# Performance work log

Measured on AMD Instinct MI355X. Metric: run time of the kernel, lower is better.

Reference implementation:

```python
import jax, jax.numpy as jnp
import numpy as np

B, T, I, H, O = 64, 2048, 128, 256, 128


def setup_inputs() -> dict:
    key = jax.random.key(0)
    ks = jax.random.split(key, 7)
    s_xh = 1.0 / np.sqrt(I)
    s_hh = 1.0 / np.sqrt(H)
    return {
        "x": jax.random.normal(ks[0], (B, T, I), dtype=jnp.float32),
        "h0": jax.random.normal(ks[1], (B, H), dtype=jnp.float32),
        "Wxh": jax.random.uniform(ks[2], (H, I), jnp.float32, -s_xh, s_xh),
        "Whh": jax.random.uniform(ks[3], (H, H), jnp.float32, -s_hh, s_hh),
        "bh": jax.random.uniform(ks[4], (H,), jnp.float32, -s_hh, s_hh),
        "Wout": jax.random.uniform(ks[5], (O, H), jnp.float32, -s_hh, s_hh),
        "bout": jax.random.uniform(ks[6], (O,), jnp.float32, -s_hh, s_hh),
    }


def reference(x, h0, Wxh, Whh, bh, Wout, bout):
    # x: (B, T, I) -> scan over time with hidden state h: (B, H)
    def step(h, xt):
        # Elman cell: h' = tanh(x Wxh^T + h Whh^T + b)
        h_new = jnp.tanh(xt @ Wxh.T + h @ Whh.T + bh)
        y = h_new @ Wout.T + bout  # (B, O) per-step output head
        return h_new, y

    xT = jnp.swapaxes(x, 0, 1)  # (T, B, I)
    hT, Ys = jax.lax.scan(step, h0, xT)
    Y = jnp.swapaxes(Ys, 0, 1)  # (B, T, O)
    return Y, hT
```

## Files before the change

### kernel.cpp

```cpp
#include <hip/hip_runtime.h>
#include <hip/hip_bf16.h>
#include <hip/hip_fp16.h>

#define B_SZ 64
#define T_SZ 2048
#define I_SZ 128
#define H_SZ 256
#define O_SZ 128

typedef _Float16 half_t;
typedef _Float16 h2_t __attribute__((ext_vector_type(2)));
typedef _Float16 h8_t __attribute__((ext_vector_type(8)));
typedef float    f4_t __attribute__((ext_vector_type(4)));

static __device__ __forceinline__ h2_t uint_as_h2(unsigned u) {
  union { unsigned u; h2_t h; } x; x.u = u; return x.h;
}
static __device__ __forceinline__ unsigned pack_h2(float a, float b) {
  h2_t h; h[0] = (_Float16)a; h[1] = (_Float16)b;
  union { h2_t h; unsigned u; } x; x.h = h; return x.u;
}
static __device__ __forceinline__ float dot2(h2_t a, h2_t b, float c) {
#if __has_builtin(__builtin_amdgcn_fdot2)
  return __builtin_amdgcn_fdot2(a, b, c, false);
#else
  return c + (float)a[0] * (float)b[0] + (float)a[1] * (float)b[1];
#endif
}
static __device__ __forceinline__ float fast_rcp(float x) {
#if __has_builtin(__builtin_amdgcn_rcpf)
  return __builtin_amdgcn_rcpf(x);
#else
  return 1.0f / x;
#endif
}

template <int BM, int BN, int BK, int KTOT, bool A_HALF, bool OUT_HALF>
__global__ __launch_bounds__(256, 2) void gemm_tn_bias(
    const void* __restrict__ Ap, const float* __restrict__ Bw,
    const float* __restrict__ bias, void* __restrict__ Out, int ldo) {
  extern __shared__ half_t lds[];
  half_t* As = lds;
  half_t* Bs = lds + BM * BK;

  const int tid = threadIdx.x;
  const long row0 = (long)blockIdx.x * BM;
  const int col0 = blockIdx.y * BN;

  constexpr int MI = 4;
  constexpr int NJ = (BN / 2) / 16;
  const int lane = tid & 63, wid = tid >> 6;
  const int wm = (wid >> 1) * 64;
  const int wn = (wid & 1) * (BN / 2);

  f4_t acc[MI][NJ];
#pragma unroll
  for (int mi = 0; mi < MI; ++mi)
#pragma unroll
    for (int nj = 0; nj < NJ; ++nj) acc[mi][nj] = (f4_t){0.f, 0.f, 0.f, 0.f};

#pragma unroll 1
  for (int kt = 0; kt < KTOT / BK; ++kt) {
    if (kt) __syncthreads();
    constexpr int AIT = (BM * BK) / (256 * 8);
#pragma unroll
    for (int it = 0; it < AIT; ++it) {
      int idx = (it * 256 + tid) * 8;
      int r = idx / BK, c = idx % BK;
      uint4 v;
      if (A_HALF) {
        v = *(const uint4*)((const half_t*)Ap + (row0 + r) * (long)KTOT +
                            kt * BK + c);
      } else {
        const float* src =
            (const float*)Ap + (row0 + r) * (long)KTOT + kt * BK + c;
        float4 f0 = *(const float4*)(src);
        float4 f1 = *(const float4*)(src + 4);
        v.x = pack_h2(f0.x, f0.y); v.y = pack_h2(f0.z, f0.w);
        v.z = pack_h2(f1.x, f1.y); v.w = pack_h2(f1.z, f1.w);
      }
      int chunk = (c >> 3) ^ (r & 7);
      *(uint4*)(&As[r * BK + chunk * 8]) = v;
    }
    constexpr int BIT = (BN * BK) / (256 * 8);
#pragma unroll
    for (int it = 0; it < BIT; ++it) {
      int idx = (it * 256 + tid) * 8;
      int r = idx / BK, c = idx % BK;
      const float* src = Bw + (long)(col0 + r) * KTOT + kt * BK + c;
      float4 f0 = *(const float4*)(src);
      float4 f1 = *(const float4*)(src + 4);
      uint4 v;
      v.x = pack_h2(f0.x, f0.y); v.y = pack_h2(f0.z, f0.w);
      v.z = pack_h2(f1.x, f1.y); v.w = pack_h2(f1.z, f1.w);
      int chunk = (c >> 3) ^ (r & 7);
      *(uint4*)(&Bs[r * BK + chunk * 8]) = v;
    }
    __syncthreads();

#pragma unroll
    for (int ks = 0; ks < BK / 32; ++ks) {
      h8_t af[MI], bf[NJ];
#pragma unroll
      for (int mi = 0; mi < MI; ++mi) {
        int r = wm + mi * 16 + (lane & 15);
        int chunk = (ks * 4 + (lane >> 4)) ^ (r & 7);
        af[mi] = *(const h8_t*)(&As[r * BK + chunk * 8]);
      }
#pragma unroll
      for (int nj = 0; nj < NJ; ++nj) {
        int r = wn + nj * 16 + (lane & 15);
        int chunk = (ks * 4 + (lane >> 4)) ^ (r & 7);
        bf[nj] = *(const h8_t*)(&Bs[r * BK + chunk * 8]);
      }
#pragma unroll
      for (int mi = 0; mi < MI; ++mi)
#pragma unroll
        for (int nj = 0; nj < NJ; ++nj)
          acc[mi][nj] = __builtin_amdgcn_mfma_f32_16x16x32_f16(
              af[mi], bf[nj], acc[mi][nj], 0, 0, 0);
    }
  }

#pragma unroll
  for (int mi = 0; mi < MI; ++mi) {
#pragma unroll
    for (int nj = 0; nj < NJ; ++nj) {
#pragma unroll
      for (int e = 0; e < 4; ++e) {
        long row = row0 + wm + mi * 16 + (lane >> 4) * 4 + e;
        int col = col0 + wn + nj * 16 + (lane & 15);
        float val = acc[mi][nj][e] + bias[col];
        if (OUT_HALF)
          ((half_t*)Out)[row * ldo + col] = (half_t)val;
        else
          ((float*)Out)[row * ldo + col] = val;
      }
    }
  }
}

__global__ __launch_bounds__(256, 1) void rnn_scan(
    const half_t* __restrict__ Xp,
    const float* __restrict__ Whh,
    const float* __restrict__ h0,
    half_t* __restrict__ Hs,
    float* __restrict__ hT) {
  __shared__ __align__(16) unsigned short hbuf[2][H_SZ];
  const int tid = threadIdx.x;
  const int b = blockIdx.x;
  const int q = tid & 3;
  const int g = tid >> 2;

  unsigned wpk[4][32];
#pragma unroll
  for (int r = 0; r < 4; ++r) {
    const float* wrow = Whh + (4 * g + r) * H_SZ + q * 64;
#pragma unroll
    for (int i = 0; i < 16; ++i) {
      float4 f = *(const float4*)(wrow + i * 4);
      wpk[r][2 * i] = pack_h2(f.x, f.y);
      wpk[r][2 * i + 1] = pack_h2(f.z, f.w);
    }
  }
  {
    union { _Float16 h; unsigned short s; } cv;
    cv.h = (_Float16)h0[b * H_SZ + tid];
    hbuf[0][tid] = cv.s;
  }
  __syncthreads();

  const half_t* xp = Xp + (long)b * T_SZ * H_SZ + tid;
  half_t* hs = Hs + (long)b * T_SZ * H_SZ + tid;
  float* hTo = hT + b * H_SZ + tid;

  half_t xv = xp[0];
#pragma unroll 1
  for (int t = 0; t < T_SZ; ++t) {
    half_t xnxt = (t + 1 < T_SZ) ? xp[(long)(t + 1) * H_SZ] : (half_t)0.0f;
    const int cur = t & 1;
    const uint4* hp = (const uint4*)(&hbuf[cur][q * 64]);
    float a0 = 0.f, a1 = 0.f, a2 = 0.f, a3 = 0.f;
#pragma unroll
    for (int i = 0; i < 8; ++i) {
      uint4 v = hp[i];
      unsigned hv0 = v.x, hv1 = v.y, hv2 = v.z, hv3 = v.w;
#define DOT_STEP(c, hvu)                                     \
  {                                                          \
    h2_t hh = uint_as_h2(hvu);                               \
    a0 = dot2(uint_as_h2(wpk[0][i * 4 + c]), hh, a0);        \
    a1 = dot2(uint_as_h2(wpk[1][i * 4 + c]), hh, a1);        \
    a2 = dot2(uint_as_h2(wpk[2][i * 4 + c]), hh, a2);        \
    a3 = dot2(uint_as_h2(wpk[3][i * 4 + c]), hh, a3);        \
  }
      DOT_STEP(0, hv0) DOT_STEP(1, hv1) DOT_STEP(2, hv2) DOT_STEP(3, hv3)
#undef DOT_STEP
    }
    a0 += __shfl_xor(a0, 1); a0 += __shfl_xor(a0, 2);
    a1 += __shfl_xor(a1, 1); a1 += __shfl_xor(a1, 2);
    a2 += __shfl_xor(a2, 1); a2 += __shfl_xor(a2, 2);
    a3 += __shfl_xor(a3, 1); a3 += __shfl_xor(a3, 2);
    float a = (q == 0) ? a0 : (q == 1) ? a1 : (q == 2) ? a2 : a3;
    a += (float)xv;
    float ex = __expf(2.0f * a);
    float hn = 1.0f - 2.0f * fast_rcp(ex + 1.0f);

    hs[(long)t * H_SZ] = (half_t)hn;
    if (t == T_SZ - 1) *hTo = hn;
    {
      union { _Float16 h; unsigned short s; } cv;
      cv.h = (_Float16)hn;
      hbuf[cur ^ 1][tid] = cv.s;
    }
    xv = xnxt;
    __syncthreads();
  }
}

extern "C" void kernel_launch(void* const* d_in, const int* in_sizes, int n_in,
                              void* d_out, int out_size, void* d_ws,
                              size_t ws_size, hipStream_t stream) {
  const float* x = (const float*)d_in[0];
  const float* h0 = (const float*)d_in[1];
  const float* Wxh = (const float*)d_in[2];
  const float* Whh = (const float*)d_in[3];
  const float* bh = (const float*)d_in[4];
  const float* Wout = (const float*)d_in[5];
  const float* bout = (const float*)d_in[6];

  half_t* Xp = (half_t*)d_out;
  half_t* Hs = (half_t*)d_ws;
  float* Y = (float*)d_out;
  float* hT = (float*)d_out + (long)B_SZ * T_SZ * O_SZ;

  const long M = (long)B_SZ * T_SZ;

  {
    dim3 grid((unsigned)(M / 128), H_SZ / 128);
    size_t sh = 2ull * 128 * 128 * sizeof(half_t);
    hipLaunchKernelGGL((gemm_tn_bias<128, 128, 128, 128, false, true>), grid,
                       dim3(256), sh, stream, (const void*)x, Wxh, bh,
                       (void*)Xp, H_SZ);
  }
  hipLaunchKernelGGL(rnn_scan, dim3(B_SZ), dim3(256), 0, stream, Xp, Whh, h0,
                     Hs, hT);
  {
    dim3 grid((unsigned)(M / 128), O_SZ / 128);
    size_t sh = 2ull * 128 * 128 * sizeof(half_t);
    hipLaunchKernelGGL((gemm_tn_bias<128, 128, 128, 256, true, false>), grid,
                       dim3(256), sh, stream, (const void*)Hs, Wout, bout,
                       (void*)Y, O_SZ);
  }
}
```

Baseline: 1.328 ms.

## Split RNN scan across 512 threads with two-way K split per output

The recurrent scan kernel now uses 512 threads per batch row. Each output neuron is computed by two lanes that each cover half of the hidden dimension, and the halves are combined with one cross-half shuffle instead of the previous four-lane group with two shuffle stages per accumulator. This shortens the per-step serial dot-product chain, which is on the latency-bound critical path. The cost is more threads per barrier and redundant tanh work on non-writer lanes. Packing to fp16 also switches to the cvt_pkrtz builtin, which rounds toward zero instead of to nearest.

```diff
diff --git a/kernel.cpp b/kernel.cpp
--- a/kernel.cpp
+++ b/kernel.cpp
@@ -10,6 +10,7 @@
 
 typedef _Float16 half_t;
 typedef _Float16 h2_t __attribute__((ext_vector_type(2)));
+typedef __fp16   fp16x2_t __attribute__((ext_vector_type(2)));
 typedef _Float16 h8_t __attribute__((ext_vector_type(8)));
 typedef float    f4_t __attribute__((ext_vector_type(4)));
 
@@ -17,8 +18,14 @@
   union { unsigned u; h2_t h; } x; x.u = u; return x.h;
 }
 static __device__ __forceinline__ unsigned pack_h2(float a, float b) {
+#if __has_builtin(__builtin_amdgcn_cvt_pkrtz)
+  union { fp16x2_t h; unsigned u; } x;
+  x.h = __builtin_amdgcn_cvt_pkrtz(a, b);
+  return x.u;
+#else
   h2_t h; h[0] = (_Float16)a; h[1] = (_Float16)b;
-  union { h2_t h; unsigned u; } x; x.h = h; return x.u;
+  union { h2_t h; unsigned u; } x2; x2.h = h; return x2.u;
+#endif
 }
 static __device__ __forceinline__ float dot2(h2_t a, h2_t b, float c) {
 #if __has_builtin(__builtin_amdgcn_fdot2)
@@ -140,7 +147,7 @@
   }
 }
 
-__global__ __launch_bounds__(256, 1) void rnn_scan(
+__global__ __launch_bounds__(512, 1) void rnn_scan(
     const half_t* __restrict__ Xp,
     const float* __restrict__ Whh,
     const float* __restrict__ h0,
@@ -149,68 +156,59 @@
   __shared__ __align__(16) unsigned short hbuf[2][H_SZ];
   const int tid = threadIdx.x;
   const int b = blockIdx.x;
-  const int q = tid & 3;
-  const int g = tid >> 2;
-
-  unsigned wpk[4][32];
-#pragma unroll
-  for (int r = 0; r < 4; ++r) {
-    const float* wrow = Whh + (4 * g + r) * H_SZ + q * 64;
-#pragma unroll
-    for (int i = 0; i < 16; ++i) {
+  const int lane = tid & 63;
+  const int w = tid >> 6;
+  const int out = w * 32 + (lane & 31);
+  const int kh = lane >> 5;
+
+  unsigned wpk[64];
+  {
+    const float* wrow = Whh + out * H_SZ + kh * 128;
+#pragma unroll
+    for (int i = 0; i < 32; ++i) {
       float4 f = *(const float4*)(wrow + i * 4);
-      wpk[r][2 * i] = pack_h2(f.x, f.y);
-      wpk[r][2 * i + 1] = pack_h2(f.z, f.w);
-    }
-  }
-  {
+      wpk[2 * i] = pack_h2(f.x, f.y);
+      wpk[2 * i + 1] = pack_h2(f.z, f.w);
+    }
+  }
+  if (tid < H_SZ) {
     union { _Float16 h; unsigned short s; } cv;
     cv.h = (_Float16)h0[b * H_SZ + tid];
     hbuf[0][tid] = cv.s;
   }
   __syncthreads();
 
-  const half_t* xp = Xp + (long)b * T_SZ * H_SZ + tid;
-  half_t* hs = Hs + (long)b * T_SZ * H_SZ + tid;
-  float* hTo = hT + b * H_SZ + tid;
+  const half_t* xp = Xp + (long)b * T_SZ * H_SZ + out;
+  half_t* hs = Hs + (long)b * T_SZ * H_SZ + out;
+  const bool writer = (kh == 0);
 
   half_t xv = xp[0];
 #pragma unroll 1
   for (int t = 0; t < T_SZ; ++t) {
     half_t xnxt = (t + 1 < T_SZ) ? xp[(long)(t + 1) * H_SZ] : (half_t)0.0f;
     const int cur = t & 1;
-    const uint4* hp = (const uint4*)(&hbuf[cur][q * 64]);
+    const uint4* hp = (const uint4*)(&hbuf[cur][kh * 128]);
     float a0 = 0.f, a1 = 0.f, a2 = 0.f, a3 = 0.f;
 #pragma unroll
-    for (int i = 0; i < 8; ++i) {
+    for (int i = 0; i < 16; ++i) {
       uint4 v = hp[i];
-      unsigned hv0 = v.x, hv1 = v.y, hv2 = v.z, hv3 = v.w;
-#define DOT_STEP(c, hvu)                                     \
-  {                                                          \
-    h2_t hh = uint_as_h2(hvu);                               \
-    a0 = dot2(uint_as_h2(wpk[0][i * 4 + c]), hh, a0);        \
-    a1 = dot2(uint_as_h2(wpk[1][i * 4 + c]), hh, a1);        \
-    a2 = dot2(uint_as_h2(wpk[2][i * 4 + c]), hh, a2);        \
-    a3 = dot2(uint_as_h2(wpk[3][i * 4 + c]), hh, a3);        \
-  }
-      DOT_STEP(0, hv0) DOT_STEP(1, hv1) DOT_STEP(2, hv2) DOT_STEP(3, hv3)
-#undef DOT_STEP
-    }
-    a0 += __shfl_xor(a0, 1); a0 += __shfl_xor(a0, 2);
-    a1 += __shfl_xor(a1, 1); a1 += __shfl_xor(a1, 2);
-    a2 += __shfl_xor(a2, 1); a2 += __shfl_xor(a2, 2);
-    a3 += __shfl_xor(a3, 1); a3 += __shfl_xor(a3, 2);
-    float a = (q == 0) ? a0 : (q == 1) ? a1 : (q == 2) ? a2 : a3;
+      a0 = dot2(uint_as_h2(wpk[4 * i + 0]), uint_as_h2(v.x), a0);
+      a1 = dot2(uint_as_h2(wpk[4 * i + 1]), uint_as_h2(v.y), a1);
+      a2 = dot2(uint_as_h2(wpk[4 * i + 2]), uint_as_h2(v.z), a2);
+      a3 = dot2(uint_as_h2(wpk[4 * i + 3]), uint_as_h2(v.w), a3);
+    }
+    float a = (a0 + a1) + (a2 + a3);
+    a += __shfl_xor(a, 32);
     a += (float)xv;
     float ex = __expf(2.0f * a);
     float hn = 1.0f - 2.0f * fast_rcp(ex + 1.0f);
 
-    hs[(long)t * H_SZ] = (half_t)hn;
-    if (t == T_SZ - 1) *hTo = hn;
-    {
+    if (writer) {
       union { _Float16 h; unsigned short s; } cv;
       cv.h = (_Float16)hn;
-      hbuf[cur ^ 1][tid] = cv.s;
+      hs[(long)t * H_SZ] = cv.h;
+      hbuf[cur ^ 1][out] = cv.s;
+      if (t == T_SZ - 1) hT[b * H_SZ + out] = hn;
     }
     xv = xnxt;
     __syncthreads();
@@ -242,7 +240,7 @@
                        dim3(256), sh, stream, (const void*)x, Wxh, bh,
                        (void*)Xp, H_SZ);
   }
-  hipLaunchKernelGGL(rnn_scan, dim3(B_SZ), dim3(256), 0, stream, Xp, Whh, h0,
+  hipLaunchKernelGGL(rnn_scan, dim3(B_SZ), dim3(512), 0, stream, Xp, Whh, h0,
                      Hs, hT);
   {
     dim3 grid((unsigned)(M / 128), O_SZ / 128);
```

Result: no change. 1.318 ms (-0.8%).
